# Kernel optimization log

Hardware: AMD Instinct MI355X
Metric: run time of the kernel (lower is better)

Reference implementation:

```python
import jax, jax.numpy as jnp
import numpy as np

B, N, FIN, H, D = 4, 2048, 128, 4, 64
ALPHA = 0.2  # LeakyReLU negative slope


def _xavier_uniform(key, shape):
    fan_in, fan_out = shape[0], shape[1]
    limit = float(np.sqrt(6.0 / (fan_in + fan_out)))
    return jax.random.uniform(key, shape, jnp.float32, -limit, limit)


def setup_inputs() -> dict:
    key = jax.random.key(0)
    k1, k2, k3, k4 = jax.random.split(key, 4)
    x = jax.random.normal(k1, (B, N, FIN), jnp.float32)
    adj = jax.random.randint(k2, (B, N, N), 0, 2, jnp.int32)  # dense 0/1 mask
    W = _xavier_uniform(k3, (FIN, H * D))
    a = _xavier_uniform(k4, (2 * D, 1))
    return {"x": x, "adj": adj, "W": W, "a": a}


def reference(x, adj, W, a):
    Bb, Nn, _ = x.shape
    Dd = a.shape[0] // 2
    Hh = W.shape[1] // Dd
    # h: [B, N, H, D]
    h = (x @ W).reshape(Bb, Nn, Hh, Dd)
    # Additive attention: e[b,i,j,h] = leakyrelu(a1 . h[b,i,h] + a2 . h[b,j,h])
    a1 = a[:Dd, 0]
    a2 = a[Dd:, 0]
    ei = jnp.einsum('bnhd,d->bnh', h, a1)  # source (row i) term
    ej = jnp.einsum('bnhd,d->bnh', h, a2)  # dest (col j) term
    e = ei[:, :, None, :] + ej[:, None, :, :]  # [B, N, N, H]
    e = jnp.where(e >= 0, e, ALPHA * e)  # LeakyReLU
    e = jnp.where(adj[..., None] == 0, -jnp.inf, e)
    att = jax.nn.softmax(e, axis=2)  # softmax over neighbors j
    # dropout is a no-op in eval mode (training=False)
    out = jnp.einsum('bijh,bjhd->bihd', att, h)  # [B, N, H, D]
    return out.mean(axis=2)  # mean over heads -> [B, N, D]
```

## Files before the change

kernel.cpp:

```cpp
#include <hip/hip_runtime.h>

#define NN 2048
#define NH 4
#define DD 64
#define FIN 128
#define NB 4
#define LOG2E 1.44269504f

typedef unsigned short u16;
typedef unsigned int u32;
typedef short sh8 __attribute__((ext_vector_type(8)));
typedef float f32x4 __attribute__((ext_vector_type(4)));

static __device__ __forceinline__ u16 f2bf(float f) {
    u32 u = __builtin_bit_cast(u32, f);
    u += 0x7fffu + ((u >> 16) & 1u);
    return (u16)(u >> 16);
}
static __device__ __forceinline__ u32 pk_bf(float a, float b) {
    u32 ua = __builtin_bit_cast(u32, a) + 0x8000u;
    u32 ub = __builtin_bit_cast(u32, b) + 0x8000u;
    return __builtin_amdgcn_perm(ub, ua, 0x07060302u);
}
static __device__ __forceinline__ float fast_exp2(float x) {
    float r;
    asm("v_exp_f32 %0, %1" : "=v"(r) : "v"(x));
    return r;
}

static __device__ __forceinline__ void cd_probe(int ln15, int q, int* irow, int* icol) {
    sh8 pa, pb, qa, qb;
    #pragma unroll
    for (int ii = 0; ii < 8; ++ii) {
        pa[ii] = (short)f2bf((float)ln15);
        pb[ii] = 0;
        qa[ii] = 0;
        qb[ii] = (short)f2bf((float)ln15);
    }
    if (q == 0) { pb[0] = (short)f2bf(1.0f); qa[0] = (short)f2bf(1.0f); }
    f32x4 z = {};
    f32x4 prow = __builtin_amdgcn_mfma_f32_16x16x32_bf16(pa, pb, z, 0, 0, 0);
    f32x4 pcol = __builtin_amdgcn_mfma_f32_16x16x32_bf16(qa, qb, z, 0, 0, 0);
    #pragma unroll
    for (int r = 0; r < 4; ++r) {
        irow[r] = (int)(prow[r] + 0.5f);
        icol[r] = (int)(pcol[r] + 0.5f);
    }
}


__global__ __launch_bounds__(256)
void k_prep(const float* __restrict__ x, const float* __restrict__ W,
            u16* __restrict__ x_bf, u16* __restrict__ WT) {
    const int bi = blockIdx.x;
    const int tid = threadIdx.x;
    if (bi < 1024) {
        const size_t idx = (size_t)bi * 1024 + tid * 4;
        const float4 v = *(const float4*)(x + idx);
        ushort4 o;
        o.x = f2bf(v.x); o.y = f2bf(v.y); o.z = f2bf(v.z); o.w = f2bf(v.w);
        *(ushort4*)(x_bf + idx) = o;
    } else {
        const int k = bi - 1024;
        WT[tid * FIN + k] = f2bf(W[k * 256 + tid]);
    }
}

__global__ __launch_bounds__(256)
void k_pack(const int* __restrict__ adj, u32* __restrict__ msk) {
    const int wid  = (blockIdx.x * 256 + threadIdx.x) >> 6;
    const int lane = threadIdx.x & 63;
    for (int t0 = wid; t0 < NB * NN * 32; t0 += 32768) {
        int av[4];
        #pragma unroll
        for (int k = 0; k < 4; ++k) {
            const int t  = t0 + k * 8192;
            const int jc = t & 31;
            const int i  = (t >> 5) & (NN - 1);
            const int b  = t >> 16;
            av[k] = adj[((size_t)(b * NN + i)) * NN + jc * 64 + lane];
        }
        #pragma unroll
        for (int k = 0; k < 4; ++k) {
            const int t  = t0 + k * 8192;
            const int jc = t & 31;
            const int i  = (t >> 5) & (NN - 1);
            const int b  = t >> 16;
            const unsigned long long m = __ballot(av[k] != 0);
            if (lane == 0) {
                msk[((size_t)(b * 64 + jc * 2 + 0)) * NN + i] = (u32)m;
                msk[((size_t)(b * 64 + jc * 2 + 1)) * NN + i] = (u32)(m >> 32);
            }
        }
    }
}

__global__ __launch_bounds__(256, 2)
void k_gemm_h(const u16* __restrict__ x_bf, const u16* __restrict__ WT,
              const float* __restrict__ a,
              u16* __restrict__ hT, float* __restrict__ ei_g, float* __restrict__ ej_g) {
    const int nb = blockIdx.x, head = blockIdx.y, b = blockIdx.z;
    const int tid = threadIdx.x, w = tid >> 6, lane = tid & 63, ln15 = lane & 15, q = lane >> 4;
    const int c0 = head * 64 + w * 16, n0 = nb * 64;

    int irow[4], icol[4];
    cd_probe(ln15, q, irow, icol);

    sh8 af[4], bf[4][4];
    #pragma unroll
    for (int ks = 0; ks < 4; ++ks)
        af[ks] = *(const sh8*)(WT + (size_t)(c0 + ln15) * FIN + ks * 32 + q * 8);
    #pragma unroll
    for (int nt = 0; nt < 4; ++nt)
        #pragma unroll
        for (int ks = 0; ks < 4; ++ks)
            bf[nt][ks] = *(const sh8*)(x_bf + ((size_t)(b * NN + n0 + nt * 16 + ln15)) * FIN + ks * 32 + q * 8);

    f32x4 acc[4] = {};
    #pragma unroll
    for (int ks = 0; ks < 4; ++ks)
        #pragma unroll
        for (int nt = 0; nt < 4; ++nt)
            acc[nt] = __builtin_amdgcn_mfma_f32_16x16x32_bf16(af[ks], bf[nt][ks], acc[nt], 0, 0, 0);

    __shared__ float cs[4][4][16][16];
    #pragma unroll
    for (int nt = 0; nt < 4; ++nt)
        #pragma unroll
        for (int r = 0; r < 4; ++r)
            cs[w][nt][irow[r]][icol[r]] = acc[nt][r];
    __syncthreads();

    const int d0 = w * 16 + 4 * q;
    float a1v[4], a2v[4];
    #pragma unroll
    for (int r = 0; r < 4; ++r) {
        a1v[r] = a[d0 + r] * LOG2E;
        a2v[r] = a[64 + d0 + r] * LOG2E;
    }

    float eip[4], ejp[4];
    #pragma unroll
    for (int nt = 0; nt < 4; ++nt) {
        float se = 0.f, sj = 0.f;
        #pragma unroll
        for (int r = 0; r < 4; ++r) {
            const float v = cs[w][nt][4 * q + r][ln15];
            hT[((size_t)(b * 256 + c0 + 4 * q + r)) * NN + n0 + nt * 16 + ln15] = f2bf(v);
            se += v * a1v[r];
            sj += v * a2v[r];
        }
        eip[nt] = se; ejp[nt] = sj;
    }
    #pragma unroll
    for (int nt = 0; nt < 4; ++nt) {
        eip[nt] += __shfl_xor(eip[nt], 16);
        eip[nt] += __shfl_xor(eip[nt], 32);
        ejp[nt] += __shfl_xor(ejp[nt], 16);
        ejp[nt] += __shfl_xor(ejp[nt], 32);
    }
    __shared__ float eis[4][64], ejs[4][64];
    if (lane < 16) {
        #pragma unroll
        for (int nt = 0; nt < 4; ++nt) {
            eis[w][nt * 16 + lane] = eip[nt];
            ejs[w][nt * 16 + lane] = ejp[nt];
        }
    }
    __syncthreads();
    if (tid < 64) {
        const float se = eis[0][tid] + eis[1][tid] + eis[2][tid] + eis[3][tid];
        const float sj = ejs[0][tid] + ejs[1][tid] + ejs[2][tid] + ejs[3][tid];
        ei_g[(size_t)(b * NH + head) * NN + n0 + tid] = se;
        ej_g[(size_t)(b * NH + head) * NN + n0 + tid] = sj;
    }
}

__global__ __launch_bounds__(256, 4)
void k_attn(const u32* __restrict__ msk, const u16* __restrict__ hT,
            const float* __restrict__ ei_g, const float* __restrict__ ej_g,
            float* __restrict__ o_part, float* __restrict__ l_part, int nj) {
    const int ib = blockIdx.x, js = blockIdx.y, b = blockIdx.z;
    const int js_n = gridDim.y;
    const int tid = threadIdx.x, hd = tid >> 6, lane = tid & 63, ln15 = lane & 15, q = lane >> 4;
    const int q8 = q * 8;
    const int iA = ib * 32 + ln15;

    int irow[4], icol[4];
    cd_probe(ln15, q, irow, icol);

    const size_t bhd = (size_t)(b * NH + hd) * NN;
    const float eivA = ei_g[bhd + iA];
    const float eivB = ei_g[bhd + iA + 16];
    const u32*   mptr = msk + (size_t)(b * 64) * NN;
    const float* ejp  = ej_g + bhd + q8;
    const u16*   hptr = hT + ((size_t)(b * 256 + hd * 64 + ln15)) * NN + q8;

    sh8 ones;
    #pragma unroll
    for (int ii = 0; ii < 8; ++ii) ones[ii] = (short)0x3F80;

    f32x4 acc[8] = {};
    f32x4 accl[2] = {};

    const int jt0 = js * nj;
    u32 mA = mptr[(size_t)jt0 * NN + iA];
    u32 mB = mptr[(size_t)jt0 * NN + iA + 16];
    float4 e0 = *(const float4*)(ejp + jt0 * 32);
    float4 e1 = *(const float4*)(ejp + jt0 * 32 + 4);

    for (int t = 0; t < nj; ++t) {
        const int jc = (jt0 + t) * 32;
        const sh8 h0 = *(const sh8*)(hptr + jc);
        const sh8 h1 = *(const sh8*)(hptr + 16 * NN + jc);
        const sh8 h2 = *(const sh8*)(hptr + 32 * NN + jc);
        const sh8 h3 = *(const sh8*)(hptr + 48 * NN + jc);

        const float ef[8] = { e0.x, e0.y, e0.z, e0.w, e1.x, e1.y, e1.z, e1.w };
        const u32 mqA = mA >> q8;
        const u32 mqB = mB >> q8;

        const int tn = (t + 1 < nj) ? (jt0 + t + 1) : jt0;
        const u32 mAn = mptr[(size_t)tn * NN + iA];
        const u32 mBn = mptr[(size_t)tn * NN + iA + 16];
        const float4 e0n = *(const float4*)(ejp + tn * 32);
        const float4 e1n = *(const float4*)(ejp + tn * 32 + 4);

        float pA[8], pB[8];
        #pragma unroll
        for (int ii = 0; ii < 8; ++ii) {
            float eA = eivA + ef[ii];
            float eB = eivB + ef[ii];
            eA = fmaxf(eA, 0.2f * eA);
            eB = fmaxf(eB, 0.2f * eB);
            const float xA = fast_exp2(eA);
            const float xB = fast_exp2(eB);
            pA[ii] = (mqA & (1u << ii)) ? xA : 0.f;
            pB[ii] = (mqB & (1u << ii)) ? xB : 0.f;
        }
        union { uint4 u; sh8 v; } avA, avB;
        avA.u.x = pk_bf(pA[0], pA[1]); avA.u.y = pk_bf(pA[2], pA[3]);
        avA.u.z = pk_bf(pA[4], pA[5]); avA.u.w = pk_bf(pA[6], pA[7]);
        avB.u.x = pk_bf(pB[0], pB[1]); avB.u.y = pk_bf(pB[2], pB[3]);
        avB.u.z = pk_bf(pB[4], pB[5]); avB.u.w = pk_bf(pB[6], pB[7]);

        acc[0] = __builtin_amdgcn_mfma_f32_16x16x32_bf16(avA.v, h0, acc[0], 0, 0, 0);
        acc[1] = __builtin_amdgcn_mfma_f32_16x16x32_bf16(avA.v, h1, acc[1], 0, 0, 0);
        acc[2] = __builtin_amdgcn_mfma_f32_16x16x32_bf16(avA.v, h2, acc[2], 0, 0, 0);
        acc[3] = __builtin_amdgcn_mfma_f32_16x16x32_bf16(avA.v, h3, acc[3], 0, 0, 0);
        accl[0] = __builtin_amdgcn_mfma_f32_16x16x32_bf16(avA.v, ones, accl[0], 0, 0, 0);
        acc[4] = __builtin_amdgcn_mfma_f32_16x16x32_bf16(avB.v, h0, acc[4], 0, 0, 0);
        acc[5] = __builtin_amdgcn_mfma_f32_16x16x32_bf16(avB.v, h1, acc[5], 0, 0, 0);
        acc[6] = __builtin_amdgcn_mfma_f32_16x16x32_bf16(avB.v, h2, acc[6], 0, 0, 0);
        acc[7] = __builtin_amdgcn_mfma_f32_16x16x32_bf16(avB.v, h3, acc[7], 0, 0, 0);
        accl[1] = __builtin_amdgcn_mfma_f32_16x16x32_bf16(avB.v, ones, accl[1], 0, 0, 0);

        mA = mAn; mB = mBn; e0 = e0n; e1 = e1n;
    }

    const size_t pbA = (((size_t)b * 128 + ib * 2 + 0) * js_n + js) * NH + hd;
    const size_t pbB = (((size_t)b * 128 + ib * 2 + 1) * js_n + js) * NH + hd;
    #pragma unroll
    for (int r = 0; r < 4; ++r) {
        l_part[pbA * 16 + irow[r]] = accl[0][r];
        l_part[pbB * 16 + irow[r]] = accl[1][r];
    }
    float* opA = o_part + pbA * 1024;
    float* opB = o_part + pbB * 1024;
    #pragma unroll
    for (int dt = 0; dt < 4; ++dt)
        #pragma unroll
        for (int r = 0; r < 4; ++r) {
            opA[(size_t)irow[r] * 64 + dt * 16 + icol[r]] = acc[dt][r];
            opB[(size_t)irow[r] * 64 + dt * 16 + icol[r]] = acc[4 + dt][r];
        }
}

__global__ __launch_bounds__(256)
void k_combine(const float* __restrict__ o_part, const float* __restrict__ l_part,
               float* __restrict__ out, int js_n) {
    const int ib = blockIdx.x, b = blockIdx.y;
    const int tid = threadIdx.x;
    const int i = tid >> 4, d4 = (tid & 15) * 4;
    float4 sacc = {0.f, 0.f, 0.f, 0.f};
    #pragma unroll
    for (int h = 0; h < NH; ++h) {
        float l = 0.f;
        float4 oh = {0.f, 0.f, 0.f, 0.f};
        for (int js = 0; js < js_n; ++js) {
            const size_t pbase = (((size_t)b * 128 + ib) * js_n + js) * NH + h;
            l += l_part[pbase * 16 + i];
            const float4 v = *(const float4*)(o_part + pbase * 1024 + (size_t)i * 64 + d4);
            oh.x += v.x; oh.y += v.y; oh.z += v.z; oh.w += v.w;
        }
        const float inv = 0.25f / l;
        sacc.x += oh.x * inv; sacc.y += oh.y * inv; sacc.z += oh.z * inv; sacc.w += oh.w * inv;
    }
    *(float4*)(out + ((size_t)(b * NN) + ib * 16 + i) * DD + d4) = sacc;
}

extern "C" void kernel_launch(void* const* d_in, const int* in_sizes, int n_in,
                              void* d_out, int out_size, void* d_ws, size_t ws_size,
                              hipStream_t stream) {
    const float* x = nullptr; const int* adj = nullptr;
    const float* W = nullptr; const float* a = nullptr;
    for (int i = 0; i < n_in; ++i) {
        switch (in_sizes[i]) {
            case NB * NN * FIN:  x   = (const float*)d_in[i]; break;
            case NB * NN * NN:   adj = (const int*)d_in[i];   break;
            case FIN * 256:      W   = (const float*)d_in[i]; break;
            case 2 * DD:         a   = (const float*)d_in[i]; break;
            default: break;
        }
    }
    if (!x)   x   = (const float*)d_in[0];
    if (!adj) adj = (const int*)d_in[1];
    if (!W)   W   = (const float*)d_in[2];
    if (!a)   a   = (const float*)d_in[3];
    float* out = (float*)d_out;

    char* ws = (char*)d_ws;
    u16*   x_bf = (u16*)(ws);
    u16*   WT   = (u16*)(ws + 2097152);
    float* ei   = (float*)(ws + 2162688);
    float* ej   = (float*)(ws + 2293760);
    u16*   hT   = (u16*)(ws + 2424832);
    u32*   msk  = (u32*)(ws + 6619136);
    float* l_p  = (float*)(ws + 8716288);
    float* o_p  = (float*)(ws + 9240576);

    const size_t need4 = 9240576 + (size_t)4 * 8388608;
    const size_t need2 = 9240576 + (size_t)2 * 8388608;
    const int js_n = (ws_size >= need4) ? 4 : (ws_size >= need2) ? 2 : 1;

    k_prep<<<dim3(1152), dim3(256), 0, stream>>>(x, W, x_bf, WT);
    k_pack<<<dim3(2048), dim3(256), 0, stream>>>(adj, msk);
    k_gemm_h<<<dim3(32, NH, NB), dim3(256), 0, stream>>>(x_bf, WT, a, hT, ei, ej);
    k_attn<<<dim3(64, js_n, NB), dim3(256), 0, stream>>>(msk, hT, ei, ej, o_p, l_p, 64 / js_n);
    k_combine<<<dim3(128, NB), dim3(256), 0, stream>>>(o_p, l_p, out, js_n);
}
```

Before: 161.5 us.

## Fuse W transpose into mask packing, convert x in-GEMM, prefetch h in attention

Drops the separate x-to-bf16 prep kernel. The W transpose is merged into the adjacency packing kernel and done through a shared-memory tile, and the projection GEMM loads fp32 x into LDS, converting to bf16 there. Each GEMM block now computes all four heads for a 64-row tile, which removes the cross-wave reduction of ei/ej. The attention loop prefetches the next h fragments alongside the mask and ej loads, with occupancy hint lowered to 3, and combine is templated on the split count so its loads can be issued up front. The trade-off is fewer but heavier GEMM blocks and higher register pressure in attention.

```diff
diff --git a/kernel.cpp b/kernel.cpp
--- a/kernel.cpp
+++ b/kernel.cpp
@@ -50,133 +50,143 @@
 
 
 __global__ __launch_bounds__(256)
-void k_prep(const float* __restrict__ x, const float* __restrict__ W,
-            u16* __restrict__ x_bf, u16* __restrict__ WT) {
-    const int bi = blockIdx.x;
+void k_pack(const int* __restrict__ adj, const float* __restrict__ W,
+            u32* __restrict__ msk, u16* __restrict__ WT) {
     const int tid = threadIdx.x;
-    if (bi < 1024) {
-        const size_t idx = (size_t)bi * 1024 + tid * 4;
-        const float4 v = *(const float4*)(x + idx);
-        ushort4 o;
-        o.x = f2bf(v.x); o.y = f2bf(v.y); o.z = f2bf(v.z); o.w = f2bf(v.w);
-        *(ushort4*)(x_bf + idx) = o;
+    if (blockIdx.x < 2048) {
+        const int wid  = (blockIdx.x * 256 + tid) >> 6;
+        const int lane = tid & 63;
+        for (int t0 = wid; t0 < NB * NN * 32; t0 += 32768) {
+            int av[4];
+            #pragma unroll
+            for (int k = 0; k < 4; ++k) {
+                const int t  = t0 + k * 8192;
+                const int jc = t & 31;
+                const int i  = (t >> 5) & (NN - 1);
+                const int b  = t >> 16;
+                av[k] = adj[((size_t)(b * NN + i)) * NN + jc * 64 + lane];
+            }
+            #pragma unroll
+            for (int k = 0; k < 4; ++k) {
+                const int t  = t0 + k * 8192;
+                const int jc = t & 31;
+                const int i  = (t >> 5) & (NN - 1);
+                const int b  = t >> 16;
+                const unsigned long long m = __ballot(av[k] != 0);
+                if (lane == 0) {
+                    msk[((size_t)(b * 64 + jc * 2 + 0)) * NN + i] = (u32)m;
+                    msk[((size_t)(b * 64 + jc * 2 + 1)) * NN + i] = (u32)(m >> 32);
+                }
+            }
+        }
     } else {
-        const int k = bi - 1024;
-        WT[tid * FIN + k] = f2bf(W[k * 256 + tid]);
+        const int bt  = blockIdx.x - 2048;
+        const int kt  = bt & 3;
+        const int ct8 = bt >> 2;
+        __shared__ float tile[32][33];
+        const int rr = tid >> 5, cc = tid & 31;
+        #pragma unroll
+        for (int i = 0; i < 4; ++i)
+            tile[rr + 8 * i][cc] = W[(size_t)(kt * 32 + rr + 8 * i) * 256 + ct8 * 32 + cc];
+        __syncthreads();
+        #pragma unroll
+        for (int i = 0; i < 4; ++i)
+            WT[(size_t)(ct8 * 32 + rr + 8 * i) * FIN + kt * 32 + cc] = f2bf(tile[cc][rr + 8 * i]);
     }
 }
 
 __global__ __launch_bounds__(256)
-void k_pack(const int* __restrict__ adj, u32* __restrict__ msk) {
-    const int wid  = (blockIdx.x * 256 + threadIdx.x) >> 6;
-    const int lane = threadIdx.x & 63;
-    for (int t0 = wid; t0 < NB * NN * 32; t0 += 32768) {
-        int av[4];
-        #pragma unroll
-        for (int k = 0; k < 4; ++k) {
-            const int t  = t0 + k * 8192;
-            const int jc = t & 31;
-            const int i  = (t >> 5) & (NN - 1);
-            const int b  = t >> 16;
-            av[k] = adj[((size_t)(b * NN + i)) * NN + jc * 64 + lane];
-        }
-        #pragma unroll
-        for (int k = 0; k < 4; ++k) {
-            const int t  = t0 + k * 8192;
-            const int jc = t & 31;
-            const int i  = (t >> 5) & (NN - 1);
-            const int b  = t >> 16;
-            const unsigned long long m = __ballot(av[k] != 0);
-            if (lane == 0) {
-                msk[((size_t)(b * 64 + jc * 2 + 0)) * NN + i] = (u32)m;
-                msk[((size_t)(b * 64 + jc * 2 + 1)) * NN + i] = (u32)(m >> 32);
-            }
-        }
-    }
-}
-
-__global__ __launch_bounds__(256, 2)
-void k_gemm_h(const u16* __restrict__ x_bf, const u16* __restrict__ WT,
+void k_gemm_h(const float* __restrict__ x, const u16* __restrict__ WT,
               const float* __restrict__ a,
               u16* __restrict__ hT, float* __restrict__ ei_g, float* __restrict__ ej_g) {
-    const int nb = blockIdx.x, head = blockIdx.y, b = blockIdx.z;
-    const int tid = threadIdx.x, w = tid >> 6, lane = tid & 63, ln15 = lane & 15, q = lane >> 4;
-    const int c0 = head * 64 + w * 16, n0 = nb * 64;
+    const int nb = blockIdx.x, b = blockIdx.y;
+    const int tid = threadIdx.x, hd = tid >> 6, lane = tid & 63, ln15 = lane & 15, q = lane >> 4;
+    const int q8 = q * 8;
+    const int n0 = nb * 64;
+
+    __shared__ u16 xs[64][136];
+    __shared__ float cs[4][4][4][16][16];
+    {
+        const int col = (tid & 31) * 4;
+        const int r0  = tid >> 5;
+        #pragma unroll
+        for (int rr = 0; rr < 8; ++rr) {
+            const int row = r0 + rr * 8;
+            const float4 v = *(const float4*)(x + ((size_t)(b * NN + n0 + row)) * FIN + col);
+            *(u32*)&xs[row][col]     = pk_bf(v.x, v.y);
+            *(u32*)&xs[row][col + 2] = pk_bf(v.z, v.w);
+        }
+    }
+    __syncthreads();
 
     int irow[4], icol[4];
     cd_probe(ln15, q, irow, icol);
 
-    sh8 af[4], bf[4][4];
-    #pragma unroll
-    for (int ks = 0; ks < 4; ++ks)
-        af[ks] = *(const sh8*)(WT + (size_t)(c0 + ln15) * FIN + ks * 32 + q * 8);
-    #pragma unroll
-    for (int nt = 0; nt < 4; ++nt)
-        #pragma unroll
-        for (int ks = 0; ks < 4; ++ks)
-            bf[nt][ks] = *(const sh8*)(x_bf + ((size_t)(b * NN + n0 + nt * 16 + ln15)) * FIN + ks * 32 + q * 8);
-
-    f32x4 acc[4] = {};
-    #pragma unroll
-    for (int ks = 0; ks < 4; ++ks)
+    f32x4 acc[4][4] = {};
+    #pragma unroll
+    for (int ks = 0; ks < 4; ++ks) {
+        sh8 af[4], bfr[4];
+        #pragma unroll
+        for (int ct = 0; ct < 4; ++ct)
+            af[ct] = *(const sh8*)(WT + (size_t)(hd * 64 + ct * 16 + ln15) * FIN + ks * 32 + q8);
         #pragma unroll
         for (int nt = 0; nt < 4; ++nt)
-            acc[nt] = __builtin_amdgcn_mfma_f32_16x16x32_bf16(af[ks], bf[nt][ks], acc[nt], 0, 0, 0);
-
-    __shared__ float cs[4][4][16][16];
-    #pragma unroll
-    for (int nt = 0; nt < 4; ++nt)
-        #pragma unroll
-        for (int r = 0; r < 4; ++r)
-            cs[w][nt][irow[r]][icol[r]] = acc[nt][r];
-    __syncthreads();
-
-    const int d0 = w * 16 + 4 * q;
-    float a1v[4], a2v[4];
-    #pragma unroll
-    for (int r = 0; r < 4; ++r) {
-        a1v[r] = a[d0 + r] * LOG2E;
-        a2v[r] = a[64 + d0 + r] * LOG2E;
-    }
-
-    float eip[4], ejp[4];
-    #pragma unroll
-    for (int nt = 0; nt < 4; ++nt) {
-        float se = 0.f, sj = 0.f;
+            bfr[nt] = *(const sh8*)&xs[nt * 16 + ln15][ks * 32 + q8];
+        #pragma unroll
+        for (int ct = 0; ct < 4; ++ct)
+            #pragma unroll
+            for (int nt = 0; nt < 4; ++nt)
+                acc[ct][nt] = __builtin_amdgcn_mfma_f32_16x16x32_bf16(af[ct], bfr[nt], acc[ct][nt], 0, 0, 0);
+    }
+
+    float a1v[4][4], a2v[4][4];
+    #pragma unroll
+    for (int ct = 0; ct < 4; ++ct)
         #pragma unroll
         for (int r = 0; r < 4; ++r) {
-            const float v = cs[w][nt][4 * q + r][ln15];
-            hT[((size_t)(b * 256 + c0 + 4 * q + r)) * NN + n0 + nt * 16 + ln15] = f2bf(v);
-            se += v * a1v[r];
-            sj += v * a2v[r];
-        }
-        eip[nt] = se; ejp[nt] = sj;
+            const int d = ct * 16 + 4 * q + r;
+            a1v[ct][r] = a[d] * LOG2E;
+            a2v[ct][r] = a[64 + d] * LOG2E;
+        }
+
+    float eip[4] = {}, ejq[4] = {};
+    #pragma unroll
+    for (int ct = 0; ct < 4; ++ct) {
+        #pragma unroll
+        for (int nt = 0; nt < 4; ++nt)
+            #pragma unroll
+            for (int r = 0; r < 4; ++r)
+                cs[hd][ct][nt][irow[r]][icol[r]] = acc[ct][nt][r];
+        #pragma unroll
+        for (int nt = 0; nt < 4; ++nt) {
+            #pragma unroll
+            for (int r = 0; r < 4; ++r) {
+                const float v = cs[hd][ct][nt][4 * q + r][ln15];
+                const int d = ct * 16 + 4 * q + r;
+                hT[((size_t)(b * 256 + hd * 64 + d)) * NN + n0 + nt * 16 + ln15] = f2bf(v);
+                eip[nt] += v * a1v[ct][r];
+                ejq[nt] += v * a2v[ct][r];
+            }
+        }
     }
     #pragma unroll
     for (int nt = 0; nt < 4; ++nt) {
         eip[nt] += __shfl_xor(eip[nt], 16);
         eip[nt] += __shfl_xor(eip[nt], 32);
-        ejp[nt] += __shfl_xor(ejp[nt], 16);
-        ejp[nt] += __shfl_xor(ejp[nt], 32);
-    }
-    __shared__ float eis[4][64], ejs[4][64];
+        ejq[nt] += __shfl_xor(ejq[nt], 16);
+        ejq[nt] += __shfl_xor(ejq[nt], 32);
+    }
     if (lane < 16) {
+        const size_t bhd = (size_t)(b * NH + hd) * NN;
         #pragma unroll
         for (int nt = 0; nt < 4; ++nt) {
-            eis[w][nt * 16 + lane] = eip[nt];
-            ejs[w][nt * 16 + lane] = ejp[nt];
-        }
-    }
-    __syncthreads();
-    if (tid < 64) {
-        const float se = eis[0][tid] + eis[1][tid] + eis[2][tid] + eis[3][tid];
-        const float sj = ejs[0][tid] + ejs[1][tid] + ejs[2][tid] + ejs[3][tid];
-        ei_g[(size_t)(b * NH + head) * NN + n0 + tid] = se;
-        ej_g[(size_t)(b * NH + head) * NN + n0 + tid] = sj;
-    }
-}
-
-__global__ __launch_bounds__(256, 4)
+            ei_g[bhd + n0 + nt * 16 + lane] = eip[nt];
+            ej_g[bhd + n0 + nt * 16 + lane] = ejq[nt];
+        }
+    }
+}
+
+__global__ __launch_bounds__(256, 3)
 void k_attn(const u32* __restrict__ msk, const u16* __restrict__ hT,
             const float* __restrict__ ei_g, const float* __restrict__ ej_g,
             float* __restrict__ o_part, float* __restrict__ l_part, int nj) {
@@ -208,24 +218,26 @@
     u32 mB = mptr[(size_t)jt0 * NN + iA + 16];
     float4 e0 = *(const float4*)(ejp + jt0 * 32);
     float4 e1 = *(const float4*)(ejp + jt0 * 32 + 4);
+    sh8 h0 = *(const sh8*)(hptr + jt0 * 32);
+    sh8 h1 = *(const sh8*)(hptr + 16 * NN + jt0 * 32);
+    sh8 h2 = *(const sh8*)(hptr + 32 * NN + jt0 * 32);
+    sh8 h3 = *(const sh8*)(hptr + 48 * NN + jt0 * 32);
 
     for (int t = 0; t < nj; ++t) {
-        const int jc = (jt0 + t) * 32;
-        const sh8 h0 = *(const sh8*)(hptr + jc);
-        const sh8 h1 = *(const sh8*)(hptr + 16 * NN + jc);
-        const sh8 h2 = *(const sh8*)(hptr + 32 * NN + jc);
-        const sh8 h3 = *(const sh8*)(hptr + 48 * NN + jc);
+        const int tn  = (t + 1 < nj) ? jt0 + t + 1 : jt0;
+        const int jcn = tn * 32;
+        const u32 mAn = mptr[(size_t)tn * NN + iA];
+        const u32 mBn = mptr[(size_t)tn * NN + iA + 16];
+        const float4 e0n = *(const float4*)(ejp + jcn);
+        const float4 e1n = *(const float4*)(ejp + jcn + 4);
+        const sh8 h0n = *(const sh8*)(hptr + jcn);
+        const sh8 h1n = *(const sh8*)(hptr + 16 * NN + jcn);
+        const sh8 h2n = *(const sh8*)(hptr + 32 * NN + jcn);
+        const sh8 h3n = *(const sh8*)(hptr + 48 * NN + jcn);
 
         const float ef[8] = { e0.x, e0.y, e0.z, e0.w, e1.x, e1.y, e1.z, e1.w };
         const u32 mqA = mA >> q8;
         const u32 mqB = mB >> q8;
-
-        const int tn = (t + 1 < nj) ? (jt0 + t + 1) : jt0;
-        const u32 mAn = mptr[(size_t)tn * NN + iA];
-        const u32 mBn = mptr[(size_t)tn * NN + iA + 16];
-        const float4 e0n = *(const float4*)(ejp + tn * 32);
-        const float4 e1n = *(const float4*)(ejp + tn * 32 + 4);
-
         float pA[8], pB[8];
         #pragma unroll
         for (int ii = 0; ii < 8; ++ii) {
@@ -256,6 +268,7 @@
         accl[1] = __builtin_amdgcn_mfma_f32_16x16x32_bf16(avB.v, ones, accl[1], 0, 0, 0);
 
         mA = mAn; mB = mBn; e0 = e0n; e1 = e1n;
+        h0 = h0n; h1 = h1n; h2 = h2n; h3 = h3n;
     }
 
     const size_t pbA = (((size_t)b * 128 + ib * 2 + 0) * js_n + js) * NH + hd;
@@ -276,25 +289,37 @@
         }
 }
 
+template <int JS>
 __global__ __launch_bounds__(256)
 void k_combine(const float* __restrict__ o_part, const float* __restrict__ l_part,
-               float* __restrict__ out, int js_n) {
+               float* __restrict__ out) {
     const int ib = blockIdx.x, b = blockIdx.y;
     const int tid = threadIdx.x;
     const int i = tid >> 4, d4 = (tid & 15) * 4;
+    float  lv[NH][JS];
+    float4 ov[NH][JS];
+    #pragma unroll
+    for (int h = 0; h < NH; ++h)
+        #pragma unroll
+        for (int js = 0; js < JS; ++js) {
+            const size_t pbase = (((size_t)b * 128 + ib) * JS + js) * NH + h;
+            lv[h][js] = l_part[pbase * 16 + i];
+            ov[h][js] = *(const float4*)(o_part + pbase * 1024 + (size_t)i * 64 + d4);
+        }
     float4 sacc = {0.f, 0.f, 0.f, 0.f};
     #pragma unroll
     for (int h = 0; h < NH; ++h) {
         float l = 0.f;
         float4 oh = {0.f, 0.f, 0.f, 0.f};
-        for (int js = 0; js < js_n; ++js) {
-            const size_t pbase = (((size_t)b * 128 + ib) * js_n + js) * NH + h;
-            l += l_part[pbase * 16 + i];
-            const float4 v = *(const float4*)(o_part + pbase * 1024 + (size_t)i * 64 + d4);
-            oh.x += v.x; oh.y += v.y; oh.z += v.z; oh.w += v.w;
+        #pragma unroll
+        for (int js = 0; js < JS; ++js) {
+            l += lv[h][js];
+            oh.x += ov[h][js].x; oh.y += ov[h][js].y;
+            oh.z += ov[h][js].z; oh.w += ov[h][js].w;
         }
         const float inv = 0.25f / l;
-        sacc.x += oh.x * inv; sacc.y += oh.y * inv; sacc.z += oh.z * inv; sacc.w += oh.w * inv;
+        sacc.x += oh.x * inv; sacc.y += oh.y * inv;
+        sacc.z += oh.z * inv; sacc.w += oh.w * inv;
     }
     *(float4*)(out + ((size_t)(b * NN) + ib * 16 + i) * DD + d4) = sacc;
 }
@@ -320,22 +345,22 @@
     float* out = (float*)d_out;
 
     char* ws = (char*)d_ws;
-    u16*   x_bf = (u16*)(ws);
-    u16*   WT   = (u16*)(ws + 2097152);
-    float* ei   = (float*)(ws + 2162688);
-    float* ej   = (float*)(ws + 2293760);
-    u16*   hT   = (u16*)(ws + 2424832);
-    u32*   msk  = (u32*)(ws + 6619136);
-    float* l_p  = (float*)(ws + 8716288);
-    float* o_p  = (float*)(ws + 9240576);
-
-    const size_t need4 = 9240576 + (size_t)4 * 8388608;
-    const size_t need2 = 9240576 + (size_t)2 * 8388608;
+    u16*   WT  = (u16*)(ws);
+    float* ei  = (float*)(ws + 65536);
+    float* ej  = (float*)(ws + 196608);
+    u16*   hT  = (u16*)(ws + 327680);
+    u32*   msk = (u32*)(ws + 4521984);
+    float* l_p = (float*)(ws + 6619136);
+    float* o_p = (float*)(ws + 7143424);
+
+    const size_t need4 = 7143424 + (size_t)4 * 8388608;
+    const size_t need2 = 7143424 + (size_t)2 * 8388608;
     const int js_n = (ws_size >= need4) ? 4 : (ws_size >= need2) ? 2 : 1;
 
-    k_prep<<<dim3(1152), dim3(256), 0, stream>>>(x, W, x_bf, WT);
-    k_pack<<<dim3(2048), dim3(256), 0, stream>>>(adj, msk);
-    k_gemm_h<<<dim3(32, NH, NB), dim3(256), 0, stream>>>(x_bf, WT, a, hT, ei, ej);
+    k_pack<<<dim3(2080), dim3(256), 0, stream>>>(adj, W, msk, WT);
+    k_gemm_h<<<dim3(32, NB), dim3(256), 0, stream>>>(x, WT, a, hT, ei, ej);
     k_attn<<<dim3(64, js_n, NB), dim3(256), 0, stream>>>(msk, hT, ei, ej, o_p, l_p, 64 / js_n);
-    k_combine<<<dim3(128, NB), dim3(256), 0, stream>>>(o_p, l_p, out, js_n);
-}
+    if (js_n == 4)      k_combine<4><<<dim3(128, NB), dim3(256), 0, stream>>>(o_p, l_p, out);
+    else if (js_n == 2) k_combine<2><<<dim3(128, NB), dim3(256), 0, stream>>>(o_p, l_p, out);
+    else                k_combine<1><<<dim3(128, NB), dim3(256), 0, stream>>>(o_p, l_p, out);
+}
```

After: 156.1 us. 3.3% less time.
